# Performance work log

Hardware: AMD Instinct MI355X
Metric: run time of the kernel (lower is better)

The kernel has to match this reference:

```python
import jax, jax.numpy as jnp
import numpy as np

B, S, D = 16, 512, 768      # batch, max_n_words, context_dim (input_size)
E, R = 128, 2048            # entities per doc, candidate relations per doc
H = 768                     # config.hidden_size
H2 = H // 2                 # 384
OUT = 2                     # binary relation classes


def _linear_params(k, fan_in, fan_out):
    k1, k2 = jax.random.split(k)
    bound = 1.0 / np.sqrt(fan_in)
    W = jax.random.uniform(k1, (fan_in, fan_out), minval=-bound, maxval=bound, dtype=jnp.float32)
    b = jax.random.uniform(k2, (fan_out,), minval=-bound, maxval=bound, dtype=jnp.float32)
    return W, b


def setup_inputs() -> dict:
    key = jax.random.key(0)
    ks = jax.random.split(key, 16)
    hW1, hb1 = _linear_params(ks[0], 2 * D, H)
    hW2, hb2 = _linear_params(ks[1], H, H2)
    tW1, tb1 = _linear_params(ks[2], 2 * D, H)
    tW2, tb2 = _linear_params(ks[3], H, H2)
    bnd = 1.0 / np.sqrt(H2)
    bil_w = jax.random.uniform(ks[4], (OUT, H2, H2), minval=-bnd, maxval=bnd, dtype=jnp.float32)
    lW, lb = _linear_params(ks[5], 2 * H2, OUT)
    emb = jax.random.normal(ks[6], (3, D), dtype=jnp.float32)  # entity_emb
    hidden_states = jax.random.normal(ks[7], (B, S, D), dtype=jnp.float32)
    ent_start = jax.random.randint(ks[8], (B, E), 0, S)
    ent_label = jax.random.randint(ks[9], (B, E), 0, 3)
    rel_head = jax.random.randint(ks[10], (B, R), 0, E)
    rel_tail = jax.random.randint(ks[11], (B, R), 0, E)
    rel_label = jax.random.randint(ks[12], (B, R), 0, 2)
    return dict(hidden_states=hidden_states, emb=emb,
                hW1=hW1, hb1=hb1, hW2=hW2, hb2=hb2,
                tW1=tW1, tb1=tb1, tW2=tW2, tb2=tb2,
                bil_w=bil_w, lW=lW, lb=lb,
                ent_start=ent_start, ent_label=ent_label,
                rel_head=rel_head, rel_tail=rel_tail, rel_label=rel_label)


def reference(hidden_states, emb, hW1, hb1, hW2, hb2, tW1, tb1, tW2, tb2,
              bil_w, lW, lb, ent_start, ent_label, rel_head, rel_tail, rel_label):
    def tower(rel_idx, W1, b1, W2, b2):
        start = jnp.take_along_axis(ent_start, rel_idx, axis=1)              # [B,R]
        lab = jnp.take_along_axis(ent_label, rel_idx, axis=1)                # [B,R]
        hid = jnp.take_along_axis(hidden_states, start[..., None], axis=1)   # [B,R,D]
        rep = jnp.concatenate([hid, emb[lab]], axis=-1)                      # [B,R,2D]
        h = jax.nn.relu(rep @ W1 + b1)                                       # [B,R,H]
        return jax.nn.relu(h @ W2 + b2)                                      # [B,R,H2]

    heads = tower(rel_head, hW1, hb1, hW2, hb2)
    tails = tower(rel_tail, tW1, tb1, tW2, tb2)
    # Biaffine: bilinear (no bias) + linear over concat
    logits = (jnp.einsum('bri,oij,brj->bro', heads, bil_w, tails)
              + jnp.concatenate([heads, tails], axis=-1) @ lW + lb)          # [B,R,2]
    logp = jax.nn.log_softmax(logits, axis=-1)
    loss = -jnp.mean(jnp.take_along_axis(logp, rel_label[..., None], axis=-1))
    return loss, logits
```

## Files before the change

kernel.cpp:

```cpp
#include <hip/hip_runtime.h>
#include <hip/hip_bf16.h>
#include <cstdint>

typedef unsigned short ushort_t;
typedef __bf16 bf16x8 __attribute__((ext_vector_type(8)));
typedef float f32x4 __attribute__((ext_vector_type(4)));

#define B_   16
#define S_   512
#define D_   768
#define E_   128
#define R_   2048
#define NREL 32768

__device__ inline ushort_t f2b(float f) {
    uint32_t u = __builtin_bit_cast(uint32_t, f);
    uint32_t r = (u + 0x7fffu + ((u >> 16) & 1u)) >> 16;
    return (ushort_t)r;
}
__device__ inline float b2f(ushort_t u) {
    uint32_t v = ((uint32_t)u) << 16;
    return __builtin_bit_cast(float, v);
}
__device__ inline float bl(uint32_t u) {
    uint32_t v = u << 16;
    return __builtin_bit_cast(float, v);
}
__device__ inline float bh(uint32_t u) {
    uint32_t v = u & 0xffff0000u;
    return __builtin_bit_cast(float, v);
}

__global__ __launch_bounds__(256) void prep_kernel(
    const float* __restrict__ hidden, const float* __restrict__ emb,
    const float* __restrict__ lW,
    const int* __restrict__ ent_start, const int* __restrict__ ent_label,
    ushort_t* __restrict__ repE, ushort_t* __restrict__ BmatT,
    ushort_t* __restrict__ lWtT, float* __restrict__ out)
{
    int idx = blockIdx.x * 256 + threadIdx.x;
    if (idx == 0) out[0] = 0.0f;
    if (idx < 786432) {
        int row = idx / 384, q = idx - row * 384;
        int c = q * 4;
        int b = row >> 7;
        int st = ent_start[row], lab = ent_label[row];
        const float* srcp = (c < 768)
            ? hidden + ((size_t)(b * S_ + st) * D_ + c)
            : emb + ((size_t)lab * D_ + (c - 768));
        float4 v = *reinterpret_cast<const float4*>(srcp);
        uint32_t lo = (uint32_t)f2b(v.x) | ((uint32_t)f2b(v.y) << 16);
        uint32_t hi = (uint32_t)f2b(v.z) | ((uint32_t)f2b(v.w) << 16);
        uint2 pk; pk.x = lo; pk.y = hi;
        *reinterpret_cast<uint2*>(repE + (size_t)idx * 4) = pk;
        return;
    }
    int i2 = idx - 786432;
    if (i2 < 768) {
        int o = i2 / 384, kk = i2 - o * 384;
        BmatT[(768 + o) * 384 + kk] = f2b(lW[kk * 2 + o]);
        return;
    }
    i2 -= 768;
    if (i2 < 768) {
        int o = i2 / 384, ii = i2 - o * 384;
        lWtT[o * 384 + ii] = f2b(lW[(384 + ii) * 2 + o]);
    }
}

__global__ __launch_bounds__(256) void transpose_w(
    const float* __restrict__ hW1, const float* __restrict__ tW1,
    const float* __restrict__ hW2, const float* __restrict__ tW2,
    const float* __restrict__ bil,
    ushort_t* __restrict__ hW1T, ushort_t* __restrict__ tW1T,
    ushort_t* __restrict__ hW2T, ushort_t* __restrict__ tW2T,
    ushort_t* __restrict__ BmatT)
{
    __shared__ float tile[32][33];
    int z = blockIdx.z;
    const float* src; ushort_t* dst; int Rr, Cc;
    switch (z) {
        case 0:  src = hW1;          dst = hW1T;           Rr = 1536; Cc = 768; break;
        case 1:  src = tW1;          dst = tW1T;           Rr = 1536; Cc = 768; break;
        case 2:  src = hW2;          dst = hW2T;           Rr = 768;  Cc = 384; break;
        case 3:  src = tW2;          dst = tW2T;           Rr = 768;  Cc = 384; break;
        case 4:  src = bil;          dst = BmatT;          Rr = 384;  Cc = 384; break;
        default: src = bil + 147456; dst = BmatT + 147456; Rr = 384;  Cc = 384; break;
    }
    int tR = blockIdx.x * 32, tC = blockIdx.y * 32;
    if (tR >= Rr || tC >= Cc) return;
    int tx = threadIdx.x & 31, ty = threadIdx.x >> 5;
#pragma unroll
    for (int r = 0; r < 4; ++r)
        tile[ty + r * 8][tx] = src[(size_t)(tR + ty + r * 8) * Cc + tC + tx];
    __syncthreads();
#pragma unroll
    for (int r = 0; r < 4; ++r)
        dst[(size_t)(tC + ty + r * 8) * Rr + tR + tx] = f2b(tile[tx][ty + r * 8]);
}

__global__ __launch_bounds__(256) void gemm_lds(
    const ushort_t* __restrict__ A0, const ushort_t* __restrict__ A1,
    const ushort_t* __restrict__ Bt0, const ushort_t* __restrict__ Bt1,
    const float* __restrict__ bias0, const float* __restrict__ bias1,
    ushort_t* __restrict__ out0, ushort_t* __restrict__ out1,
    int M, int N, int K, int doRelu)
{
    __shared__ ushort_t As[64 * 32];
    __shared__ ushort_t Bs[64 * 32];
    const ushort_t* A   = blockIdx.z ? A1 : A0;
    const ushort_t* Bt  = blockIdx.z ? Bt1 : Bt0;
    const float*   bias = blockIdx.z ? bias1 : bias0;
    ushort_t*      out  = blockIdx.z ? out1 : out0;

    int t = threadIdx.x;
    int lane = t & 63, wave = t >> 6;
    int tileM = blockIdx.x * 64, tileN = blockIdx.y * 64;
    int wm = (wave >> 1) * 32, wn = (wave & 1) * 32;
    int l15 = lane & 15, quad = lane >> 4;

    const ushort_t* gA = A  + (size_t)tileM * K;
    const ushort_t* gB = Bt + (size_t)tileN * K;

    int srow = t >> 2, sc8 = (t & 3) << 3;

    f32x4 acc[2][2];
#pragma unroll
    for (int a = 0; a < 2; ++a)
#pragma unroll
        for (int b = 0; b < 2; ++b) {
            acc[a][b][0] = 0.f; acc[a][b][1] = 0.f;
            acc[a][b][2] = 0.f; acc[a][b][3] = 0.f;
        }

    for (int k0 = 0; k0 < K; k0 += 32) {
        __builtin_amdgcn_global_load_lds(
            (const __attribute__((address_space(1))) void*)(gA + (size_t)srow * K + k0 + sc8),
            (__attribute__((address_space(3))) void*)(As + t * 8), 16, 0, 0);
        __builtin_amdgcn_global_load_lds(
            (const __attribute__((address_space(1))) void*)(gB + (size_t)srow * K + k0 + sc8),
            (__attribute__((address_space(3))) void*)(Bs + t * 8), 16, 0, 0);
        __syncthreads();
        bf16x8 af[2], bfr[2];
#pragma unroll
        for (int mi = 0; mi < 2; ++mi)
            af[mi] = *reinterpret_cast<const bf16x8*>(As + (wm + mi * 16 + l15) * 32 + quad * 8);
#pragma unroll
        for (int ni = 0; ni < 2; ++ni)
            bfr[ni] = *reinterpret_cast<const bf16x8*>(Bs + (wn + ni * 16 + l15) * 32 + quad * 8);
#pragma unroll
        for (int mi = 0; mi < 2; ++mi)
#pragma unroll
            for (int ni = 0; ni < 2; ++ni)
                acc[mi][ni] = __builtin_amdgcn_mfma_f32_16x16x32_bf16(af[mi], bfr[ni], acc[mi][ni], 0, 0, 0);
        __syncthreads();
    }

#pragma unroll
    for (int mi = 0; mi < 2; ++mi) {
        int gr = tileM + wm + mi * 16 + quad * 4;
#pragma unroll
        for (int ni = 0; ni < 2; ++ni) {
            int gc = tileN + wn + ni * 16 + l15;
            if (gc < N) {
                float bb = bias ? bias[gc] : 0.0f;
#pragma unroll
                for (int r = 0; r < 4; ++r) {
                    float v = acc[mi][ni][r] + bb;
                    if (doRelu) v = fmaxf(v, 0.0f);
                    out[(size_t)(gr + r) * N + gc] = f2b(v);
                }
            }
        }
    }
}

__global__ __launch_bounds__(256) void rel_kernel(
    const ushort_t* __restrict__ Uext, const ushort_t* __restrict__ tailsE,
    const ushort_t* __restrict__ lWtT, const float* __restrict__ lb,
    const int* __restrict__ rel_head, const int* __restrict__ rel_tail,
    const int* __restrict__ rel_label, float* __restrict__ out)
{
    __shared__ float wsum[4];
    int lane = threadIdx.x & 63, wave = threadIdx.x >> 6;
    const uint32_t* lw32 = reinterpret_cast<const uint32_t*>(lWtT);
    float lb0 = lb[0], lb1 = lb[1];
    float lossAcc = 0.0f;
    int base = (blockIdx.x * 4 + wave) * 8;

    for (int q = 0; q < 8; ++q) {
        int rel = base + q;
        int b = rel >> 11;
        int h = rel_head[rel], t = rel_tail[rel], lab = rel_label[rel];
        const uint32_t* uh = reinterpret_cast<const uint32_t*>(Uext + (size_t)(b * E_ + h) * 770);
        const uint32_t* tv = reinterpret_cast<const uint32_t*>(tailsE + (size_t)(b * E_ + t) * 384);

        float a0 = 0.f, a1 = 0.f, w0s = 0.f, w1s = 0.f;
#pragma unroll
        for (int j = 0; j < 3; ++j) {
            int i = lane + 64 * j;
            uint32_t tu = tv[i];
            uint32_t u0 = uh[i], u1 = uh[192 + i];
            uint32_t q0 = lw32[i], q1 = lw32[192 + i];
            float tl = bl(tu), th = bh(tu);
            a0  += tl * bl(u0) + th * bh(u0);
            a1  += tl * bl(u1) + th * bh(u1);
            w0s += tl * bl(q0) + th * bh(q0);
            w1s += tl * bl(q1) + th * bh(q1);
        }
#pragma unroll
        for (int d = 1; d < 64; d <<= 1) {
            a0  += __shfl_xor(a0, d);
            a1  += __shfl_xor(a1, d);
            w0s += __shfl_xor(w0s, d);
            w1s += __shfl_xor(w1s, d);
        }
        const ushort_t* uhs = reinterpret_cast<const ushort_t*>(uh);
        float l0v = a0 + w0s + b2f(uhs[768]) + lb0;
        float l1v = a1 + w1s + b2f(uhs[769]) + lb1;
        if (lane == 0) {
            out[1 + 2 * rel]     = l0v;
            out[1 + 2 * rel + 1] = l1v;
        }
        float m = fmaxf(l0v, l1v);
        float lse = m + logf(expf(l0v - m) + expf(l1v - m));
        lossAcc += lse - (lab ? l1v : l0v);
    }
    if (lane == 0) wsum[wave] = lossAcc;
    __syncthreads();
    if (threadIdx.x == 0) {
        float s = wsum[0] + wsum[1] + wsum[2] + wsum[3];
        atomicAdd(out, s * (1.0f / 32768.0f));
    }
}

extern "C" void kernel_launch(void* const* d_in, const int* in_sizes, int n_in,
                              void* d_out, int out_size, void* d_ws, size_t ws_size,
                              hipStream_t stream)
{
    const float* hidden = (const float*)d_in[0];
    const float* emb    = (const float*)d_in[1];
    const float* hW1    = (const float*)d_in[2];
    const float* hb1    = (const float*)d_in[3];
    const float* hW2    = (const float*)d_in[4];
    const float* hb2    = (const float*)d_in[5];
    const float* tW1    = (const float*)d_in[6];
    const float* tb1    = (const float*)d_in[7];
    const float* tW2    = (const float*)d_in[8];
    const float* tb2    = (const float*)d_in[9];
    const float* bil    = (const float*)d_in[10];
    const float* lW     = (const float*)d_in[11];
    const float* lb     = (const float*)d_in[12];
    const int* ent_start = (const int*)d_in[13];
    const int* ent_label = (const int*)d_in[14];
    const int* rel_head  = (const int*)d_in[15];
    const int* rel_tail  = (const int*)d_in[16];
    const int* rel_label = (const int*)d_in[17];
    float* out = (float*)d_out;

    char* ws = (char*)d_ws;
    ushort_t* repE   = (ushort_t*)(ws + 0);
    ushort_t* hW1T   = (ushort_t*)(ws + 6291456);
    ushort_t* tW1T   = (ushort_t*)(ws + 8650752);
    ushort_t* hW2T   = (ushort_t*)(ws + 11010048);
    ushort_t* tW2T   = (ushort_t*)(ws + 11599872);
    ushort_t* BmatT  = (ushort_t*)(ws + 12189696);
    ushort_t* lWtT   = (ushort_t*)(ws + 12781056);
    ushort_t* h1     = (ushort_t*)(ws + 12782592);
    ushort_t* t1     = (ushort_t*)(ws + 15928320);
    ushort_t* headsE = (ushort_t*)(ws + 19074048);
    ushort_t* tailsE = (ushort_t*)(ws + 20646912);
    ushort_t* Uext   = (ushort_t*)(ws + 22219776);

    prep_kernel<<<3078, 256, 0, stream>>>(
        hidden, emb, lW, ent_start, ent_label, repE, BmatT, lWtT, out);

    transpose_w<<<dim3(48, 24, 6), 256, 0, stream>>>(
        hW1, tW1, hW2, tW2, bil, hW1T, tW1T, hW2T, tW2T, BmatT);

    gemm_lds<<<dim3(32, 12, 2), 256, 0, stream>>>(
        repE, repE, hW1T, tW1T, hb1, tb1, h1, t1, 2048, 768, 1536, 1);

    gemm_lds<<<dim3(32, 6, 2), 256, 0, stream>>>(
        h1, t1, hW2T, tW2T, hb2, tb2, headsE, tailsE, 2048, 384, 768, 1);

    gemm_lds<<<dim3(32, 13, 1), 256, 0, stream>>>(
        headsE, headsE, BmatT, BmatT, nullptr, nullptr, Uext, Uext, 2048, 770, 384, 0);

    rel_kernel<<<1024, 256, 0, stream>>>(
        Uext, tailsE, lWtT, lb, rel_head, rel_tail, rel_label, out);
}
```

Baseline: 180.3 us.

## Fuse all stages into one cooperative persistent kernel with grid syncs

Merges the six launches (prep, weight transpose, three GEMMs, relation scoring) into a single cooperative kernel that uses grid-wide barriers between stages and a grid sized by occupancy. It also precomputes the tail-side linear term per entity, so the per-relation pass does less work, and it packs four relations per wave using 16-lane groups. This is meant to remove launch gaps and redundant per-relation dot products. In exchange it adds grid.sync costs and a fixed persistent grid, which can lower per-stage parallelism compared with the larger separate grids.

```diff
diff --git a/kernel.cpp b/kernel.cpp
--- a/kernel.cpp
+++ b/kernel.cpp
@@ -1,6 +1,9 @@
 #include <hip/hip_runtime.h>
 #include <hip/hip_bf16.h>
+#include <hip/hip_cooperative_groups.h>
 #include <cstdint>
+
+namespace cg = cooperative_groups;
 
 typedef unsigned short ushort_t;
 typedef __bf16 bf16x8 __attribute__((ext_vector_type(8)));
@@ -10,8 +13,6 @@
 #define S_   512
 #define D_   768
 #define E_   128
-#define R_   2048
-#define NREL 32768
 
 __device__ inline ushort_t f2b(float f) {
     uint32_t u = __builtin_bit_cast(uint32_t, f);
@@ -31,98 +32,24 @@
     return __builtin_bit_cast(float, v);
 }
 
-__global__ __launch_bounds__(256) void prep_kernel(
-    const float* __restrict__ hidden, const float* __restrict__ emb,
-    const float* __restrict__ lW,
-    const int* __restrict__ ent_start, const int* __restrict__ ent_label,
-    ushort_t* __restrict__ repE, ushort_t* __restrict__ BmatT,
-    ushort_t* __restrict__ lWtT, float* __restrict__ out)
+union SMem {
+    float tp[32][33];
+    struct { ushort_t As[64 * 32]; ushort_t Bs[64 * 32]; } g;
+};
+
+__device__ __forceinline__ void gemm_unit(
+    const ushort_t* __restrict__ A, const ushort_t* __restrict__ Bt,
+    const float* __restrict__ bias, ushort_t* __restrict__ outp,
+    int tileM, int tileN, int N, int K, int doRelu,
+    ushort_t* As, ushort_t* Bs, int t)
 {
-    int idx = blockIdx.x * 256 + threadIdx.x;
-    if (idx == 0) out[0] = 0.0f;
-    if (idx < 786432) {
-        int row = idx / 384, q = idx - row * 384;
-        int c = q * 4;
-        int b = row >> 7;
-        int st = ent_start[row], lab = ent_label[row];
-        const float* srcp = (c < 768)
-            ? hidden + ((size_t)(b * S_ + st) * D_ + c)
-            : emb + ((size_t)lab * D_ + (c - 768));
-        float4 v = *reinterpret_cast<const float4*>(srcp);
-        uint32_t lo = (uint32_t)f2b(v.x) | ((uint32_t)f2b(v.y) << 16);
-        uint32_t hi = (uint32_t)f2b(v.z) | ((uint32_t)f2b(v.w) << 16);
-        uint2 pk; pk.x = lo; pk.y = hi;
-        *reinterpret_cast<uint2*>(repE + (size_t)idx * 4) = pk;
-        return;
-    }
-    int i2 = idx - 786432;
-    if (i2 < 768) {
-        int o = i2 / 384, kk = i2 - o * 384;
-        BmatT[(768 + o) * 384 + kk] = f2b(lW[kk * 2 + o]);
-        return;
-    }
-    i2 -= 768;
-    if (i2 < 768) {
-        int o = i2 / 384, ii = i2 - o * 384;
-        lWtT[o * 384 + ii] = f2b(lW[(384 + ii) * 2 + o]);
-    }
-}
-
-__global__ __launch_bounds__(256) void transpose_w(
-    const float* __restrict__ hW1, const float* __restrict__ tW1,
-    const float* __restrict__ hW2, const float* __restrict__ tW2,
-    const float* __restrict__ bil,
-    ushort_t* __restrict__ hW1T, ushort_t* __restrict__ tW1T,
-    ushort_t* __restrict__ hW2T, ushort_t* __restrict__ tW2T,
-    ushort_t* __restrict__ BmatT)
-{
-    __shared__ float tile[32][33];
-    int z = blockIdx.z;
-    const float* src; ushort_t* dst; int Rr, Cc;
-    switch (z) {
-        case 0:  src = hW1;          dst = hW1T;           Rr = 1536; Cc = 768; break;
-        case 1:  src = tW1;          dst = tW1T;           Rr = 1536; Cc = 768; break;
-        case 2:  src = hW2;          dst = hW2T;           Rr = 768;  Cc = 384; break;
-        case 3:  src = tW2;          dst = tW2T;           Rr = 768;  Cc = 384; break;
-        case 4:  src = bil;          dst = BmatT;          Rr = 384;  Cc = 384; break;
-        default: src = bil + 147456; dst = BmatT + 147456; Rr = 384;  Cc = 384; break;
-    }
-    int tR = blockIdx.x * 32, tC = blockIdx.y * 32;
-    if (tR >= Rr || tC >= Cc) return;
-    int tx = threadIdx.x & 31, ty = threadIdx.x >> 5;
-#pragma unroll
-    for (int r = 0; r < 4; ++r)
-        tile[ty + r * 8][tx] = src[(size_t)(tR + ty + r * 8) * Cc + tC + tx];
-    __syncthreads();
-#pragma unroll
-    for (int r = 0; r < 4; ++r)
-        dst[(size_t)(tC + ty + r * 8) * Rr + tR + tx] = f2b(tile[tx][ty + r * 8]);
-}
-
-__global__ __launch_bounds__(256) void gemm_lds(
-    const ushort_t* __restrict__ A0, const ushort_t* __restrict__ A1,
-    const ushort_t* __restrict__ Bt0, const ushort_t* __restrict__ Bt1,
-    const float* __restrict__ bias0, const float* __restrict__ bias1,
-    ushort_t* __restrict__ out0, ushort_t* __restrict__ out1,
-    int M, int N, int K, int doRelu)
-{
-    __shared__ ushort_t As[64 * 32];
-    __shared__ ushort_t Bs[64 * 32];
-    const ushort_t* A   = blockIdx.z ? A1 : A0;
-    const ushort_t* Bt  = blockIdx.z ? Bt1 : Bt0;
-    const float*   bias = blockIdx.z ? bias1 : bias0;
-    ushort_t*      out  = blockIdx.z ? out1 : out0;
-
-    int t = threadIdx.x;
     int lane = t & 63, wave = t >> 6;
-    int tileM = blockIdx.x * 64, tileN = blockIdx.y * 64;
     int wm = (wave >> 1) * 32, wn = (wave & 1) * 32;
     int l15 = lane & 15, quad = lane >> 4;
-
-    const ushort_t* gA = A  + (size_t)tileM * K;
+    int srow = t >> 2, sc8 = (t & 3) << 3;
+
+    const ushort_t* gA = A + (size_t)tileM * K;
     const ushort_t* gB = Bt + (size_t)tileN * K;
-
-    int srow = t >> 2, sc8 = (t & 3) << 3;
 
     f32x4 acc[2][2];
 #pragma unroll
@@ -168,70 +95,181 @@
                 for (int r = 0; r < 4; ++r) {
                     float v = acc[mi][ni][r] + bb;
                     if (doRelu) v = fmaxf(v, 0.0f);
-                    out[(size_t)(gr + r) * N + gc] = f2b(v);
+                    outp[(size_t)(gr + r) * N + gc] = f2b(v);
                 }
             }
         }
     }
 }
 
-__global__ __launch_bounds__(256) void rel_kernel(
-    const ushort_t* __restrict__ Uext, const ushort_t* __restrict__ tailsE,
-    const ushort_t* __restrict__ lWtT, const float* __restrict__ lb,
+__global__ __launch_bounds__(256) void mega_kernel(
+    const float* __restrict__ hidden, const float* __restrict__ emb,
+    const float* __restrict__ hW1, const float* __restrict__ hb1,
+    const float* __restrict__ hW2, const float* __restrict__ hb2,
+    const float* __restrict__ tW1, const float* __restrict__ tb1,
+    const float* __restrict__ tW2, const float* __restrict__ tb2,
+    const float* __restrict__ bil, const float* __restrict__ lW,
+    const float* __restrict__ lb,
+    const int* __restrict__ ent_start, const int* __restrict__ ent_label,
     const int* __restrict__ rel_head, const int* __restrict__ rel_tail,
-    const int* __restrict__ rel_label, float* __restrict__ out)
+    const int* __restrict__ rel_label,
+    float* __restrict__ out, char* __restrict__ ws)
 {
+    __shared__ SMem sm;
     __shared__ float wsum[4];
-    int lane = threadIdx.x & 63, wave = threadIdx.x >> 6;
-    const uint32_t* lw32 = reinterpret_cast<const uint32_t*>(lWtT);
+
+    cg::grid_group grid = cg::this_grid();
+    const int bx = blockIdx.x, t = threadIdx.x;
+    const int G = gridDim.x;
+    const int lane = t & 63, wave = t >> 6;
+
+    ushort_t* repE   = (ushort_t*)(ws + 0);
+    ushort_t* hW1T   = (ushort_t*)(ws + 6291456);
+    ushort_t* tW1T   = (ushort_t*)(ws + 8650752);
+    ushort_t* hW2T   = (ushort_t*)(ws + 11010048);
+    ushort_t* tW2T   = (ushort_t*)(ws + 11599872);
+    ushort_t* BmatT  = (ushort_t*)(ws + 12189696);
+    ushort_t* lWtT   = (ushort_t*)(ws + 12781056);
+    ushort_t* h1     = (ushort_t*)(ws + 12782592);
+    ushort_t* t1     = (ushort_t*)(ws + 15928320);
+    ushort_t* headsE = (ushort_t*)(ws + 19074048);
+    ushort_t* tailsE = (ushort_t*)(ws + 20646912);
+    ushort_t* Uext   = (ushort_t*)(ws + 22219776);
+    float*    tailLin= (float*)   (ws + 25373696);
+
+    if (bx == 0 && t == 0) out[0] = 0.0f;
+    for (int u = bx; u < 6246; u += G) {
+        if (u < 3072) {
+            int idx = u * 256 + t;
+            int row = idx / 384, q = idx - row * 384;
+            int c = q * 4;
+            int b = row >> 7;
+            int st = ent_start[row], lab = ent_label[row];
+            const float* srcp = (c < 768)
+                ? hidden + ((size_t)(b * S_ + st) * D_ + c)
+                : emb + ((size_t)lab * D_ + (c - 768));
+            float4 v = *reinterpret_cast<const float4*>(srcp);
+            uint32_t lo = (uint32_t)f2b(v.x) | ((uint32_t)f2b(v.y) << 16);
+            uint32_t hi = (uint32_t)f2b(v.z) | ((uint32_t)f2b(v.w) << 16);
+            uint2 pk; pk.x = lo; pk.y = hi;
+            *reinterpret_cast<uint2*>(repE + (size_t)idx * 4) = pk;
+        } else if (u < 6240) {
+            int u2 = u - 3072;
+            const float* src; ushort_t* dst; int Rr, Cc, base;
+            if (u2 < 1152)      { src = hW1;          dst = hW1T;           Rr = 1536; Cc = 768; base = 0; }
+            else if (u2 < 2304) { src = tW1;          dst = tW1T;           Rr = 1536; Cc = 768; base = 1152; }
+            else if (u2 < 2592) { src = hW2;          dst = hW2T;           Rr = 768;  Cc = 384; base = 2304; }
+            else if (u2 < 2880) { src = tW2;          dst = tW2T;           Rr = 768;  Cc = 384; base = 2592; }
+            else if (u2 < 3024) { src = bil;          dst = BmatT;          Rr = 384;  Cc = 384; base = 2880; }
+            else                { src = bil + 147456; dst = BmatT + 147456; Rr = 384;  Cc = 384; base = 3024; }
+            int local = u2 - base, nC = Cc >> 5;
+            int tR = (local / nC) * 32, tC = (local - (local / nC) * nC) * 32;
+            int tx = t & 31, ty = t >> 5;
+#pragma unroll
+            for (int r = 0; r < 4; ++r)
+                sm.tp[ty + r * 8][tx] = src[(size_t)(tR + ty + r * 8) * Cc + tC + tx];
+            __syncthreads();
+#pragma unroll
+            for (int r = 0; r < 4; ++r)
+                dst[(size_t)(tC + ty + r * 8) * Rr + tR + tx] = f2b(sm.tp[tx][ty + r * 8]);
+            __syncthreads();
+        } else {
+            int i2 = (u - 6240) * 256 + t;
+            if (i2 < 768) {
+                int o = i2 / 384, kk = i2 - o * 384;
+                BmatT[(768 + o) * 384 + kk] = f2b(lW[kk * 2 + o]);
+            } else if (i2 < 1536) {
+                int j = i2 - 768;
+                int o = j / 384, ii = j - o * 384;
+                lWtT[o * 384 + ii] = f2b(lW[(384 + ii) * 2 + o]);
+            }
+        }
+    }
+    grid.sync();
+
+    for (int u = bx; u < 768; u += G) {
+        int z = (u >= 384);
+        int r = u - (z ? 384 : 0);
+        gemm_unit(repE, z ? tW1T : hW1T, z ? tb1 : hb1, z ? t1 : h1,
+                  (r & 31) * 64, (r >> 5) * 64, 768, 1536, 1, sm.g.As, sm.g.Bs, t);
+    }
+    grid.sync();
+
+    for (int u = bx; u < 384; u += G) {
+        int z = (u >= 192);
+        int r = u - (z ? 192 : 0);
+        gemm_unit(z ? t1 : h1, z ? tW2T : hW2T, z ? tb2 : hb2, z ? tailsE : headsE,
+                  (r & 31) * 64, (r >> 5) * 64, 384, 768, 1, sm.g.As, sm.g.Bs, t);
+    }
+    grid.sync();
+
+    for (int u = bx; u < 448; u += G) {
+        if (u < 416) {
+            gemm_unit(headsE, BmatT, nullptr, Uext,
+                      (u & 31) * 64, (u >> 5) * 64, 770, 384, 0, sm.g.As, sm.g.Bs, t);
+        } else {
+            int w = u - 416;
+            int r = w * 64 + (t >> 2), q = t & 3;
+            const uint32_t* tv = reinterpret_cast<const uint32_t*>(tailsE + (size_t)r * 384);
+            const uint32_t* lw = reinterpret_cast<const uint32_t*>(lWtT);
+            float p0 = 0.f, p1 = 0.f;
+#pragma unroll 8
+            for (int i = q * 48; i < q * 48 + 48; ++i) {
+                uint32_t tu = tv[i];
+                float tl = bl(tu), th = bh(tu);
+                uint32_t l0 = lw[i], l1 = lw[192 + i];
+                p0 += tl * bl(l0) + th * bh(l0);
+                p1 += tl * bl(l1) + th * bh(l1);
+            }
+            p0 += __shfl_xor(p0, 1); p0 += __shfl_xor(p0, 2);
+            p1 += __shfl_xor(p1, 1); p1 += __shfl_xor(p1, 2);
+            if (q == 0) tailLin[2 * r]     = p0;
+            if (q == 1) tailLin[2 * r + 1] = p1;
+        }
+    }
+    grid.sync();
+
     float lb0 = lb[0], lb1 = lb[1];
     float lossAcc = 0.0f;
-    int base = (blockIdx.x * 4 + wave) * 8;
-
-    for (int q = 0; q < 8; ++q) {
-        int rel = base + q;
+    int l = lane & 15, g = lane >> 4;
+    for (int u = bx * 4 + wave; u < 8192; u += G * 4) {
+        int rel = u * 4 + g;
         int b = rel >> 11;
-        int h = rel_head[rel], t = rel_tail[rel], lab = rel_label[rel];
+        int h = rel_head[rel], tt = rel_tail[rel], lab = rel_label[rel];
         const uint32_t* uh = reinterpret_cast<const uint32_t*>(Uext + (size_t)(b * E_ + h) * 770);
-        const uint32_t* tv = reinterpret_cast<const uint32_t*>(tailsE + (size_t)(b * E_ + t) * 384);
-
-        float a0 = 0.f, a1 = 0.f, w0s = 0.f, w1s = 0.f;
-#pragma unroll
-        for (int j = 0; j < 3; ++j) {
-            int i = lane + 64 * j;
+        const uint32_t* tv = reinterpret_cast<const uint32_t*>(tailsE + (size_t)(b * E_ + tt) * 384);
+        float a0 = 0.f, a1 = 0.f;
+#pragma unroll
+        for (int j = 0; j < 12; ++j) {
+            int i = l + 16 * j;
             uint32_t tu = tv[i];
+            float tl = bl(tu), th = bh(tu);
             uint32_t u0 = uh[i], u1 = uh[192 + i];
-            uint32_t q0 = lw32[i], q1 = lw32[192 + i];
-            float tl = bl(tu), th = bh(tu);
-            a0  += tl * bl(u0) + th * bh(u0);
-            a1  += tl * bl(u1) + th * bh(u1);
-            w0s += tl * bl(q0) + th * bh(q0);
-            w1s += tl * bl(q1) + th * bh(q1);
-        }
-#pragma unroll
-        for (int d = 1; d < 64; d <<= 1) {
-            a0  += __shfl_xor(a0, d);
-            a1  += __shfl_xor(a1, d);
-            w0s += __shfl_xor(w0s, d);
-            w1s += __shfl_xor(w1s, d);
-        }
-        const ushort_t* uhs = reinterpret_cast<const ushort_t*>(uh);
-        float l0v = a0 + w0s + b2f(uhs[768]) + lb0;
-        float l1v = a1 + w1s + b2f(uhs[769]) + lb1;
-        if (lane == 0) {
+            a0 += tl * bl(u0) + th * bh(u0);
+            a1 += tl * bl(u1) + th * bh(u1);
+        }
+#pragma unroll
+        for (int d = 1; d < 16; d <<= 1) {
+            a0 += __shfl_xor(a0, d);
+            a1 += __shfl_xor(a1, d);
+        }
+        if (l == 0) {
+            const ushort_t* uhs = reinterpret_cast<const ushort_t*>(uh);
+            int te = b * E_ + tt;
+            float l0v = a0 + tailLin[2 * te]     + b2f(uhs[768]) + lb0;
+            float l1v = a1 + tailLin[2 * te + 1] + b2f(uhs[769]) + lb1;
             out[1 + 2 * rel]     = l0v;
             out[1 + 2 * rel + 1] = l1v;
-        }
-        float m = fmaxf(l0v, l1v);
-        float lse = m + logf(expf(l0v - m) + expf(l1v - m));
-        lossAcc += lse - (lab ? l1v : l0v);
-    }
+            float m = fmaxf(l0v, l1v);
+            lossAcc += m + logf(expf(l0v - m) + expf(l1v - m)) - (lab ? l1v : l0v);
+        }
+    }
+    lossAcc += __shfl_xor(lossAcc, 16);
+    lossAcc += __shfl_xor(lossAcc, 32);
     if (lane == 0) wsum[wave] = lossAcc;
     __syncthreads();
-    if (threadIdx.x == 0) {
-        float s = wsum[0] + wsum[1] + wsum[2] + wsum[3];
-        atomicAdd(out, s * (1.0f / 32768.0f));
-    }
+    if (t == 0)
+        atomicAdd(out, (wsum[0] + wsum[1] + wsum[2] + wsum[3]) * (1.0f / 32768.0f));
 }
 
 extern "C" void kernel_launch(void* const* d_in, const int* in_sizes, int n_in,
@@ -257,36 +295,21 @@
     const int* rel_tail  = (const int*)d_in[16];
     const int* rel_label = (const int*)d_in[17];
     float* out = (float*)d_out;
-
     char* ws = (char*)d_ws;
-    ushort_t* repE   = (ushort_t*)(ws + 0);
-    ushort_t* hW1T   = (ushort_t*)(ws + 6291456);
-    ushort_t* tW1T   = (ushort_t*)(ws + 8650752);
-    ushort_t* hW2T   = (ushort_t*)(ws + 11010048);
-    ushort_t* tW2T   = (ushort_t*)(ws + 11599872);
-    ushort_t* BmatT  = (ushort_t*)(ws + 12189696);
-    ushort_t* lWtT   = (ushort_t*)(ws + 12781056);
-    ushort_t* h1     = (ushort_t*)(ws + 12782592);
-    ushort_t* t1     = (ushort_t*)(ws + 15928320);
-    ushort_t* headsE = (ushort_t*)(ws + 19074048);
-    ushort_t* tailsE = (ushort_t*)(ws + 20646912);
-    ushort_t* Uext   = (ushort_t*)(ws + 22219776);
-
-    prep_kernel<<<3078, 256, 0, stream>>>(
-        hidden, emb, lW, ent_start, ent_label, repE, BmatT, lWtT, out);
-
-    transpose_w<<<dim3(48, 24, 6), 256, 0, stream>>>(
-        hW1, tW1, hW2, tW2, bil, hW1T, tW1T, hW2T, tW2T, BmatT);
-
-    gemm_lds<<<dim3(32, 12, 2), 256, 0, stream>>>(
-        repE, repE, hW1T, tW1T, hb1, tb1, h1, t1, 2048, 768, 1536, 1);
-
-    gemm_lds<<<dim3(32, 6, 2), 256, 0, stream>>>(
-        h1, t1, hW2T, tW2T, hb2, tb2, headsE, tailsE, 2048, 384, 768, 1);
-
-    gemm_lds<<<dim3(32, 13, 1), 256, 0, stream>>>(
-        headsE, headsE, BmatT, BmatT, nullptr, nullptr, Uext, Uext, 2048, 770, 384, 0);
-
-    rel_kernel<<<1024, 256, 0, stream>>>(
-        Uext, tailsE, lWtT, lb, rel_head, rel_tail, rel_label, out);
-}
+
+    int maxB = 0;
+    if (hipOccupancyMaxActiveBlocksPerMultiprocessor(&maxB, mega_kernel, 256, 0)
+            != hipSuccess || maxB < 1)
+        maxB = 1;
+    int perCU = maxB < 4 ? maxB : 4;
+    dim3 grid(perCU * 256);
+
+    void* args[] = {
+        (void*)&hidden, (void*)&emb, (void*)&hW1, (void*)&hb1, (void*)&hW2, (void*)&hb2,
+        (void*)&tW1, (void*)&tb1, (void*)&tW2, (void*)&tb2, (void*)&bil, (void*)&lW,
+        (void*)&lb, (void*)&ent_start, (void*)&ent_label, (void*)&rel_head,
+        (void*)&rel_tail, (void*)&rel_label, (void*)&out, (void*)&ws
+    };
+    hipLaunchCooperativeKernel((void*)mega_kernel, grid, dim3(256),
+                               args, 0, stream);
+}
```

Result: slower. 372.6 us (+106.7%).
